# Performance work log

Hardware: AMD Instinct MI355X
Metric: run time of the kernel (lower is better)

The kernel has to match this reference:

```python
import jax, jax.numpy as jnp
import numpy as np

E, T, IN, OUT = 8, 16384, 1024, 1024  # n_groups, total_tokens, in_features, out_features


def setup_inputs() -> dict:
    key = jax.random.key(0)
    kx, kw, ks = jax.random.split(key, 3)
    x = jax.random.normal(kx, (T, IN), dtype=jnp.float32)
    # kaiming_uniform-ish scale for weight [E, OUT, IN]
    weight = jax.random.normal(kw, (E, OUT, IN), dtype=jnp.float32) * (1.0 / np.sqrt(IN))
    # ragged segment lengths that sum exactly to T (random cut points)
    cuts = jnp.sort(jax.random.randint(ks, (E - 1,), 0, T + 1)).astype(jnp.int32)
    seg_lens = jnp.diff(
        jnp.concatenate([jnp.zeros((1,), jnp.int32), cuts, jnp.full((1,), T, jnp.int32)])
    )
    return {"x": x, "weight": weight, "seg_lens": seg_lens}


def reference(x, weight, seg_lens):
    # Grouped GEMM: row t of x is multiplied by weight[g(t)].T where g(t) is the
    # segment (expert) that token t falls into per seg_lens. trans_b=True.
    n_groups = weight.shape[0]
    bounds = jnp.cumsum(seg_lens)                                  # [E]
    seg_id = jnp.searchsorted(bounds, jnp.arange(x.shape[0]), side="right")  # [T]
    y = jnp.zeros((x.shape[0], weight.shape[1]), dtype=x.dtype)
    for e in range(n_groups):  # small fixed loop over groups
        y = y + jnp.where((seg_id == e)[:, None], x @ weight[e].T, 0)
    return y
```

## Files before the change

### kernel.cpp

```cpp
#include <hip/hip_runtime.h>

#define T_TOK  16384
#define IN_F   1024
#define OUT_F  1024
#define NE     8
#define BM     128
#define BN     128
#define BK     32
#define NTHREADS 256
#define ROW_TILE_SLOTS 136

typedef __bf16 bf16;
typedef bf16  bf16x4 __attribute__((ext_vector_type(4)));
typedef bf16  bf16x8 __attribute__((ext_vector_type(8)));
typedef float f32x4  __attribute__((ext_vector_type(4)));

#define NX_ELEM ((size_t)T_TOK * IN_F)
#define NW_ELEM ((size_t)NE * OUT_F * IN_F)
#define WS_NEED ((NX_ELEM + NW_ELEM) * sizeof(bf16))

__global__ __launch_bounds__(NTHREADS)
void cvt_to_bf16(const float* __restrict__ x, const float* __restrict__ w,
                 bf16* __restrict__ xb, bf16* __restrict__ wb)
{
    const size_t NX8 = NX_ELEM / 8;
    const size_t NW8 = NW_ELEM / 8;
    size_t stride = (size_t)gridDim.x * blockDim.x;
    for (size_t i = (size_t)blockIdx.x * blockDim.x + threadIdx.x;
         i < NX8 + NW8; i += stride) {
        const float* src;
        bf16* dst;
        if (i < NX8) { src = x + i * 8;          dst = xb + i * 8; }
        else         { src = w + (i - NX8) * 8;  dst = wb + (i - NX8) * 8; }
        f32x4 v0 = *(const f32x4*)(src);
        f32x4 v1 = *(const f32x4*)(src + 4);
        bf16x8 h;
        #pragma unroll
        for (int j = 0; j < 4; ++j) { h[j] = (bf16)v0[j]; h[4 + j] = (bf16)v1[j]; }
        *(bf16x8*)dst = h;
    }
}

__global__ __launch_bounds__(NTHREADS)
void grouped_gemm_bf16(const bf16* __restrict__ x,
                       const bf16* __restrict__ wgt,
                       const int*  __restrict__ seg_lens,
                       float* __restrict__ out)
{
    __shared__ __align__(16) bf16 As[BM * BK];
    __shared__ __align__(16) bf16 Bs[BN * BK];

    const int m    = blockIdx.y;
    const int col0 = blockIdx.x * BN;

    int e_sel = -1, row0 = 0, rows = 0;
    {
        int start = 0, acct = 0;
        #pragma unroll
        for (int e = 0; e < NE; ++e) {
            int len = seg_lens[e];
            int nt  = (len + BM - 1) >> 7;
            if (e_sel < 0 && m >= acct && m < acct + nt) {
                e_sel = e;
                row0  = start + (m - acct) * BM;
                int rem = start + len - row0;
                rows = rem < BM ? rem : BM;
            }
            acct  += nt;
            start += len;
        }
    }
    if (e_sel < 0) return;

    const int tid  = threadIdx.x;
    const int lane = tid & 63;
    const int wave = tid >> 6;
    const int wm   = (wave >> 1) * 64;
    const int wn   = (wave & 1) * 64;
    const int quad = lane >> 4;
    const int l16  = lane & 15;

    const bf16* wbase = wgt + ((size_t)e_sel * OUT_F + (size_t)col0) * IN_F;

    f32x4 acc[4][4] = {};

    for (int k0 = 0; k0 < IN_F; k0 += BK) {
        __syncthreads();

        #pragma unroll
        for (int t = 0; t < 2; ++t) {
            int c  = t * NTHREADS + tid;
            int rg = row0 + (c >> 2);
            if (rg > T_TOK - 1) rg = T_TOK - 1;
            const bf16* gp = x + (size_t)rg * IN_F + k0 + (c & 3) * 8;
            __builtin_amdgcn_global_load_lds(
                (const __attribute__((address_space(1))) void*)gp,
                (__attribute__((address_space(3))) void*)(&As[c * 8]),
                16, 0, 0);
        }
        #pragma unroll
        for (int t = 0; t < 2; ++t) {
            int c = t * NTHREADS + tid;
            const bf16* gp = wbase + (size_t)(c >> 2) * IN_F + k0 + (c & 3) * 8;
            __builtin_amdgcn_global_load_lds(
                (const __attribute__((address_space(1))) void*)gp,
                (__attribute__((address_space(3))) void*)(&Bs[c * 8]),
                16, 0, 0);
        }
        __syncthreads();

        bf16x8 af[4], bfr[4];
        #pragma unroll
        for (int t = 0; t < 4; ++t)
            af[t] = *(const bf16x8*)(&As[(wm + t * 16 + l16) * BK + quad * 8]);
        #pragma unroll
        for (int u = 0; u < 4; ++u)
            bfr[u] = *(const bf16x8*)(&Bs[(wn + u * 16 + l16) * BK + quad * 8]);

        #pragma unroll
        for (int t = 0; t < 4; ++t)
            #pragma unroll
            for (int u = 0; u < 4; ++u)
                acc[t][u] = __builtin_amdgcn_mfma_f32_16x16x32_bf16(
                    af[t], bfr[u], acc[t][u], 0, 0, 0);
    }

    #pragma unroll
    for (int t = 0; t < 4; ++t) {
        #pragma unroll
        for (int r = 0; r < 4; ++r) {
            int row = wm + t * 16 + quad * 4 + r;
            if (row < rows) {
                size_t ob = (size_t)(row0 + row) * OUT_F + col0;
                #pragma unroll
                for (int u = 0; u < 4; ++u)
                    out[ob + wn + u * 16 + l16] = acc[t][u][r];
            }
        }
    }
}

__global__ __launch_bounds__(NTHREADS)
void grouped_gemm_f32io_fused(const float* __restrict__ x,
                              const float* __restrict__ wgt,
                              const int*  __restrict__ seg_lens,
                              float* __restrict__ out)
{
    __shared__ __align__(16) bf16 As[BM * BK];
    __shared__ __align__(16) bf16 Bs[BN * BK];

    const int m    = blockIdx.y;
    const int col0 = blockIdx.x * BN;

    int e_sel = -1, row0 = 0, rows = 0;
    {
        int start = 0, acct = 0;
        #pragma unroll
        for (int e = 0; e < NE; ++e) {
            int len = seg_lens[e];
            int nt  = (len + BM - 1) >> 7;
            if (e_sel < 0 && m >= acct && m < acct + nt) {
                e_sel = e;
                row0  = start + (m - acct) * BM;
                int rem = start + len - row0;
                rows = rem < BM ? rem : BM;
            }
            acct  += nt;
            start += len;
        }
    }
    if (e_sel < 0) return;

    const int tid  = threadIdx.x;
    const int lane = tid & 63;
    const int wave = tid >> 6;
    const int wm   = (wave >> 1) * 64;
    const int wn   = (wave & 1) * 64;
    const int quad = lane >> 4;
    const int l16  = lane & 15;

    const float* wbase = wgt + ((size_t)e_sel * OUT_F + (size_t)col0) * IN_F;

    f32x4 acc[4][4] = {};

    for (int k0 = 0; k0 < IN_F; k0 += BK) {
        f32x4 a_st[4], b_st[4];
        #pragma unroll
        for (int t = 0; t < 4; ++t) {
            int c  = t * NTHREADS + tid;
            int rg = row0 + (c >> 3);
            if (rg > T_TOK - 1) rg = T_TOK - 1;
            a_st[t] = *(const f32x4*)(x + (size_t)rg * IN_F + k0 + (c & 7) * 4);
            b_st[t] = *(const f32x4*)(wbase + (size_t)(c >> 3) * IN_F + k0 + (c & 7) * 4);
        }
        __syncthreads();
        #pragma unroll
        for (int t = 0; t < 4; ++t) {
            int c = t * NTHREADS + tid;
            bf16x4 ha, hb;
            #pragma unroll
            for (int j = 0; j < 4; ++j) { ha[j] = (bf16)a_st[t][j]; hb[j] = (bf16)b_st[t][j]; }
            *(bf16x4*)(&As[(c >> 3) * BK + (c & 7) * 4]) = ha;
            *(bf16x4*)(&Bs[(c >> 3) * BK + (c & 7) * 4]) = hb;
        }
        __syncthreads();

        bf16x8 af[4], bfr[4];
        #pragma unroll
        for (int t = 0; t < 4; ++t)
            af[t] = *(const bf16x8*)(&As[(wm + t * 16 + l16) * BK + quad * 8]);
        #pragma unroll
        for (int u = 0; u < 4; ++u)
            bfr[u] = *(const bf16x8*)(&Bs[(wn + u * 16 + l16) * BK + quad * 8]);

        #pragma unroll
        for (int t = 0; t < 4; ++t)
            #pragma unroll
            for (int u = 0; u < 4; ++u)
                acc[t][u] = __builtin_amdgcn_mfma_f32_16x16x32_bf16(
                    af[t], bfr[u], acc[t][u], 0, 0, 0);
    }

    #pragma unroll
    for (int t = 0; t < 4; ++t) {
        #pragma unroll
        for (int r = 0; r < 4; ++r) {
            int row = wm + t * 16 + quad * 4 + r;
            if (row < rows) {
                size_t ob = (size_t)(row0 + row) * OUT_F + col0;
                #pragma unroll
                for (int u = 0; u < 4; ++u)
                    out[ob + wn + u * 16 + l16] = acc[t][u][r];
            }
        }
    }
}

extern "C" void kernel_launch(void* const* d_in, const int* in_sizes, int n_in,
                              void* d_out, int out_size, void* d_ws, size_t ws_size,
                              hipStream_t stream) {
    const float* x   = (const float*)d_in[0];
    const float* wgt = (const float*)d_in[1];
    const int*   seg = (const int*)d_in[2];
    float* out = (float*)d_out;

    dim3 block(NTHREADS, 1, 1);
    dim3 grid2(OUT_F / BN, ROW_TILE_SLOTS, 1);

    if (ws_size >= WS_NEED) {
        bf16* xb = (bf16*)d_ws;
        bf16* wb = xb + NX_ELEM;
        cvt_to_bf16<<<3072, block, 0, stream>>>(x, wgt, xb, wb);
        grouped_gemm_bf16<<<grid2, block, 0, stream>>>(xb, wb, seg, out);
    } else {
        grouped_gemm_f32io_fused<<<grid2, block, 0, stream>>>(x, wgt, seg, out);
    }
}
```

Baseline: 217.5 us.

## Convert only weights to bf16 and double-buffer GEMM with in-kernel x conversion

The separate x-to-bf16 pre-pass is dropped, so only the weights are converted in a standalone kernel. The GEMM now reads fp32 x directly, converts it in registers and writes it to LDS. Both A and B tiles are double-buffered so the next tile's global loads overlap the current MFMA work, with one barrier per iteration instead of two. This removes a full 64MB read/32MB write pass over x, but x tiles are now reloaded as fp32 by each of the 8 column blocks, and per-thread register pressure rises.

```diff
diff --git a/kernel.cpp b/kernel.cpp
--- a/kernel.cpp
+++ b/kernel.cpp
@@ -7,6 +7,7 @@
 #define BM     128
 #define BN     128
 #define BK     32
+#define NITER  (IN_F / BK)
 #define NTHREADS 256
 #define ROW_TILE_SLOTS 136
 
@@ -15,40 +16,29 @@
 typedef bf16  bf16x8 __attribute__((ext_vector_type(8)));
 typedef float f32x4  __attribute__((ext_vector_type(4)));
 
-#define NX_ELEM ((size_t)T_TOK * IN_F)
 #define NW_ELEM ((size_t)NE * OUT_F * IN_F)
-#define WS_NEED ((NX_ELEM + NW_ELEM) * sizeof(bf16))
+#define WS_NEED (NW_ELEM * sizeof(bf16))
 
 __global__ __launch_bounds__(NTHREADS)
-void cvt_to_bf16(const float* __restrict__ x, const float* __restrict__ w,
-                 bf16* __restrict__ xb, bf16* __restrict__ wb)
+void cvt_w_bf16(const float* __restrict__ w, bf16* __restrict__ wb)
 {
-    const size_t NX8 = NX_ELEM / 8;
-    const size_t NW8 = NW_ELEM / 8;
-    size_t stride = (size_t)gridDim.x * blockDim.x;
-    for (size_t i = (size_t)blockIdx.x * blockDim.x + threadIdx.x;
-         i < NX8 + NW8; i += stride) {
-        const float* src;
-        bf16* dst;
-        if (i < NX8) { src = x + i * 8;          dst = xb + i * 8; }
-        else         { src = w + (i - NX8) * 8;  dst = wb + (i - NX8) * 8; }
-        f32x4 v0 = *(const f32x4*)(src);
-        f32x4 v1 = *(const f32x4*)(src + 4);
-        bf16x8 h;
-        #pragma unroll
-        for (int j = 0; j < 4; ++j) { h[j] = (bf16)v0[j]; h[4 + j] = (bf16)v1[j]; }
-        *(bf16x8*)dst = h;
-    }
+    size_t i = ((size_t)blockIdx.x * NTHREADS + threadIdx.x) * 8;
+    f32x4 v0 = *(const f32x4*)(w + i);
+    f32x4 v1 = *(const f32x4*)(w + i + 4);
+    bf16x8 h;
+    #pragma unroll
+    for (int j = 0; j < 4; ++j) { h[j] = (bf16)v0[j]; h[4 + j] = (bf16)v1[j]; }
+    *(bf16x8*)(wb + i) = h;
 }
 
 __global__ __launch_bounds__(NTHREADS)
-void grouped_gemm_bf16(const bf16* __restrict__ x,
-                       const bf16* __restrict__ wgt,
+void grouped_gemm_pipe(const float* __restrict__ x,
+                       const bf16* __restrict__ wb,
                        const int*  __restrict__ seg_lens,
                        float* __restrict__ out)
 {
-    __shared__ __align__(16) bf16 As[BM * BK];
-    __shared__ __align__(16) bf16 Bs[BN * BK];
+    __shared__ __align__(16) bf16 As[2][BM * BK];
+    __shared__ __align__(16) bf16 Bs[2][BN * BK];
 
     const int m    = blockIdx.y;
     const int col0 = blockIdx.x * BN;
@@ -80,42 +70,67 @@
     const int quad = lane >> 4;
     const int l16  = lane & 15;
 
-    const bf16* wbase = wgt + ((size_t)e_sel * OUT_F + (size_t)col0) * IN_F;
-
-    f32x4 acc[4][4] = {};
-
-    for (int k0 = 0; k0 < IN_F; k0 += BK) {
-        __syncthreads();
-
+    const int rowA = tid >> 1;
+    const int koff = (tid & 1) * 16;
+    int rgA = row0 + rowA;
+    if (rgA > T_TOK - 1) rgA = T_TOK - 1;
+    const float* aptr = x + (size_t)rgA * IN_F + koff;
+    const int aoff = rowA * BK + koff;
+
+    const bf16* wbase = wb + ((size_t)e_sel * OUT_F + col0) * IN_F;
+
+    {
+        f32x4 a0 = *(const f32x4*)(aptr + 0);
+        f32x4 a1 = *(const f32x4*)(aptr + 4);
+        f32x4 a2 = *(const f32x4*)(aptr + 8);
+        f32x4 a3 = *(const f32x4*)(aptr + 12);
         #pragma unroll
         for (int t = 0; t < 2; ++t) {
-            int c  = t * NTHREADS + tid;
-            int rg = row0 + (c >> 2);
-            if (rg > T_TOK - 1) rg = T_TOK - 1;
-            const bf16* gp = x + (size_t)rg * IN_F + k0 + (c & 3) * 8;
+            int c = t * NTHREADS + tid;
+            const bf16* gp = wbase + (size_t)(c >> 2) * IN_F + (c & 3) * 8;
             __builtin_amdgcn_global_load_lds(
                 (const __attribute__((address_space(1))) void*)gp,
-                (__attribute__((address_space(3))) void*)(&As[c * 8]),
+                (__attribute__((address_space(3))) void*)(&Bs[0][c * 8]),
                 16, 0, 0);
         }
+        bf16x8 h0, h1;
+        #pragma unroll
+        for (int j = 0; j < 4; ++j) {
+            h0[j] = (bf16)a0[j]; h0[4 + j] = (bf16)a1[j];
+            h1[j] = (bf16)a2[j]; h1[4 + j] = (bf16)a3[j];
+        }
+        *(bf16x8*)(&As[0][aoff])     = h0;
+        *(bf16x8*)(&As[0][aoff + 8]) = h1;
+    }
+
+    f32x4 acc[4][4] = {};
+
+    for (int i = 0; i < NITER; ++i) {
+        __syncthreads();
+        const int cur = i & 1, nxt = cur ^ 1;
+        const int kn  = ((i + 1) & (NITER - 1)) * BK;
+
+        f32x4 a0 = *(const f32x4*)(aptr + kn);
+        f32x4 a1 = *(const f32x4*)(aptr + kn + 4);
+        f32x4 a2 = *(const f32x4*)(aptr + kn + 8);
+        f32x4 a3 = *(const f32x4*)(aptr + kn + 12);
         #pragma unroll
         for (int t = 0; t < 2; ++t) {
             int c = t * NTHREADS + tid;
-            const bf16* gp = wbase + (size_t)(c >> 2) * IN_F + k0 + (c & 3) * 8;
+            const bf16* gp = wbase + (size_t)(c >> 2) * IN_F + kn + (c & 3) * 8;
             __builtin_amdgcn_global_load_lds(
                 (const __attribute__((address_space(1))) void*)gp,
-                (__attribute__((address_space(3))) void*)(&Bs[c * 8]),
+                (__attribute__((address_space(3))) void*)(&Bs[nxt][c * 8]),
                 16, 0, 0);
         }
-        __syncthreads();
 
         bf16x8 af[4], bfr[4];
         #pragma unroll
         for (int t = 0; t < 4; ++t)
-            af[t] = *(const bf16x8*)(&As[(wm + t * 16 + l16) * BK + quad * 8]);
+            af[t] = *(const bf16x8*)(&As[cur][(wm + t * 16 + l16) * BK + quad * 8]);
         #pragma unroll
         for (int u = 0; u < 4; ++u)
-            bfr[u] = *(const bf16x8*)(&Bs[(wn + u * 16 + l16) * BK + quad * 8]);
+            bfr[u] = *(const bf16x8*)(&Bs[cur][(wn + u * 16 + l16) * BK + quad * 8]);
 
         #pragma unroll
         for (int t = 0; t < 4; ++t)
@@ -123,6 +138,15 @@
             for (int u = 0; u < 4; ++u)
                 acc[t][u] = __builtin_amdgcn_mfma_f32_16x16x32_bf16(
                     af[t], bfr[u], acc[t][u], 0, 0, 0);
+
+        bf16x8 h0, h1;
+        #pragma unroll
+        for (int j = 0; j < 4; ++j) {
+            h0[j] = (bf16)a0[j]; h0[4 + j] = (bf16)a1[j];
+            h1[j] = (bf16)a2[j]; h1[4 + j] = (bf16)a3[j];
+        }
+        *(bf16x8*)(&As[nxt][aoff])     = h0;
+        *(bf16x8*)(&As[nxt][aoff + 8]) = h1;
     }
 
     #pragma unroll
@@ -248,10 +272,9 @@
     dim3 grid2(OUT_F / BN, ROW_TILE_SLOTS, 1);
 
     if (ws_size >= WS_NEED) {
-        bf16* xb = (bf16*)d_ws;
-        bf16* wb = xb + NX_ELEM;
-        cvt_to_bf16<<<3072, block, 0, stream>>>(x, wgt, xb, wb);
-        grouped_gemm_bf16<<<grid2, block, 0, stream>>>(xb, wb, seg, out);
+        bf16* wb = (bf16*)d_ws;
+        cvt_w_bf16<<<(int)(NW_ELEM / 8 / NTHREADS), block, 0, stream>>>(wgt, wb);
+        grouped_gemm_pipe<<<grid2, block, 0, stream>>>(x, wb, seg, out);
     } else {
         grouped_gemm_f32io_fused<<<grid2, block, 0, stream>>>(x, wgt, seg, out);
     }
```

Result: slower. 227.2 us (+4.4%).

## Restructure bf16 grouped GEMM: 64-row tiles, A direct-to-register, double-buffered swizzled B

Applied to the files above, without the earlier changes.

The bf16 GEMM kernel now uses 64-row tiles (more blocks, less padding waste on ragged segments). The A operand is loaded straight from global memory into registers in MFMA fragment layout, and the B operand is double-buffered in LDS with an XOR swizzle. The next K-slice is prefetched while the current one is computed, which leaves one barrier per iteration instead of two. Smaller tiles raise the global traffic per FLOP and halve MFMA work per wave, and the A loads skip LDS reuse, so each wave reads A rows on its own.

```diff
diff --git a/kernel.cpp b/kernel.cpp
--- a/kernel.cpp
+++ b/kernel.cpp
@@ -4,11 +4,12 @@
 #define IN_F   1024
 #define OUT_F  1024
 #define NE     8
-#define BM     128
+#define BM     64
 #define BN     128
 #define BK     32
+#define NITER  (IN_F / BK)
 #define NTHREADS 256
-#define ROW_TILE_SLOTS 136
+#define ROW_TILE_SLOTS (T_TOK / BM + NE)
 
 typedef __bf16 bf16;
 typedef bf16  bf16x4 __attribute__((ext_vector_type(4)));
@@ -42,13 +43,12 @@
 }
 
 __global__ __launch_bounds__(NTHREADS)
-void grouped_gemm_bf16(const bf16* __restrict__ x,
-                       const bf16* __restrict__ wgt,
-                       const int*  __restrict__ seg_lens,
-                       float* __restrict__ out)
+void grouped_gemm_v6(const bf16* __restrict__ xb,
+                     const bf16* __restrict__ wb,
+                     const int*  __restrict__ seg_lens,
+                     float* __restrict__ out)
 {
-    __shared__ __align__(16) bf16 As[BM * BK];
-    __shared__ __align__(16) bf16 Bs[BN * BK];
+    __shared__ __align__(16) bf16 Bs[2][BN * BK];
 
     const int m    = blockIdx.y;
     const int col0 = blockIdx.x * BN;
@@ -59,12 +59,133 @@
         #pragma unroll
         for (int e = 0; e < NE; ++e) {
             int len = seg_lens[e];
-            int nt  = (len + BM - 1) >> 7;
+            int nt  = (len + BM - 1) >> 6;
             if (e_sel < 0 && m >= acct && m < acct + nt) {
                 e_sel = e;
                 row0  = start + (m - acct) * BM;
                 int rem = start + len - row0;
                 rows = rem < BM ? rem : BM;
+            }
+            acct  += nt;
+            start += len;
+        }
+    }
+    if (e_sel < 0) return;
+
+    const int tid  = threadIdx.x;
+    const int lane = tid & 63;
+    const int wave = tid >> 6;
+    const int wm   = (wave >> 1) * 32;
+    const int wn   = (wave & 1) * 64;
+    const int quad = lane >> 4;
+    const int l16  = lane & 15;
+
+    const bf16* agp[2];
+    #pragma unroll
+    for (int t = 0; t < 2; ++t) {
+        int rg = row0 + wm + t * 16 + l16;
+        if (rg > T_TOK - 1) rg = T_TOK - 1;
+        agp[t] = xb + (size_t)rg * IN_F + quad * 8;
+    }
+
+    const bf16* bgp[2];
+    int ldsoff[2];
+    #pragma unroll
+    for (int t = 0; t < 2; ++t) {
+        int c    = t * NTHREADS + tid;
+        int rowB = c >> 2;
+        int q    = (c & 3) ^ ((rowB >> 1) & 3);
+        bgp[t]    = wb + ((size_t)e_sel * OUT_F + col0 + rowB) * IN_F + q * 8;
+        ldsoff[t] = c * 8;
+    }
+
+    int boff[4];
+    #pragma unroll
+    for (int u = 0; u < 4; ++u) {
+        int row = wn + u * 16 + l16;
+        boff[u] = row * BK + ((quad ^ ((row >> 1) & 3)) * 8);
+    }
+
+    bf16x8 apf[2];
+    apf[0] = *(const bf16x8*)(agp[0]);
+    apf[1] = *(const bf16x8*)(agp[1]);
+    #pragma unroll
+    for (int t = 0; t < 2; ++t)
+        __builtin_amdgcn_global_load_lds(
+            (const __attribute__((address_space(1))) void*)bgp[t],
+            (__attribute__((address_space(3))) void*)(&Bs[0][ldsoff[t]]),
+            16, 0, 0);
+
+    f32x4 acc[2][4] = {};
+
+    for (int i = 0; i < NITER; ++i) {
+        __syncthreads();
+        const int cur = i & 1, nxt = cur ^ 1;
+        const int kn  = ((i + 1) & (NITER - 1)) * BK;
+
+        bf16x8 a0 = apf[0], a1 = apf[1];
+
+        apf[0] = *(const bf16x8*)(agp[0] + kn);
+        apf[1] = *(const bf16x8*)(agp[1] + kn);
+        #pragma unroll
+        for (int t = 0; t < 2; ++t)
+            __builtin_amdgcn_global_load_lds(
+                (const __attribute__((address_space(1))) void*)(bgp[t] + kn),
+                (__attribute__((address_space(3))) void*)(&Bs[nxt][ldsoff[t]]),
+                16, 0, 0);
+
+        bf16x8 bfr[4];
+        #pragma unroll
+        for (int u = 0; u < 4; ++u)
+            bfr[u] = *(const bf16x8*)(&Bs[cur][boff[u]]);
+
+        #pragma unroll
+        for (int u = 0; u < 4; ++u) {
+            acc[0][u] = __builtin_amdgcn_mfma_f32_16x16x32_bf16(a0, bfr[u], acc[0][u], 0, 0, 0);
+            acc[1][u] = __builtin_amdgcn_mfma_f32_16x16x32_bf16(a1, bfr[u], acc[1][u], 0, 0, 0);
+        }
+    }
+
+    #pragma unroll
+    for (int t = 0; t < 2; ++t) {
+        #pragma unroll
+        for (int r = 0; r < 4; ++r) {
+            int row = wm + t * 16 + quad * 4 + r;
+            if (row < rows) {
+                size_t ob = (size_t)(row0 + row) * OUT_F + col0;
+                #pragma unroll
+                for (int u = 0; u < 4; ++u)
+                    out[ob + wn + u * 16 + l16] = acc[t][u][r];
+            }
+        }
+    }
+}
+
+#define FBM 128
+__global__ __launch_bounds__(NTHREADS)
+void grouped_gemm_f32io_fused(const float* __restrict__ x,
+                              const float* __restrict__ wgt,
+                              const int*  __restrict__ seg_lens,
+                              float* __restrict__ out)
+{
+    __shared__ __align__(16) bf16 As[FBM * BK];
+    __shared__ __align__(16) bf16 Bsf[BN * BK];
+
+    const int m    = blockIdx.y;
+    const int col0 = blockIdx.x * BN;
+
+    int e_sel = -1, row0 = 0, rows = 0;
+    {
+        int start = 0, acct = 0;
+        #pragma unroll
+        for (int e = 0; e < NE; ++e) {
+            int len = seg_lens[e];
+            int nt  = (len + FBM - 1) >> 7;
+            if (e_sel < 0 && m >= acct && m < acct + nt) {
+                e_sel = e;
+                row0  = start + (m - acct) * FBM;
+                int rem = start + len - row0;
+                rows = rem < FBM ? rem : FBM;
             }
             acct  += nt;
             start += len;
@@ -80,32 +201,29 @@
     const int quad = lane >> 4;
     const int l16  = lane & 15;
 
-    const bf16* wbase = wgt + ((size_t)e_sel * OUT_F + (size_t)col0) * IN_F;
+    const float* wbase = wgt + ((size_t)e_sel * OUT_F + (size_t)col0) * IN_F;
 
     f32x4 acc[4][4] = {};
 
     for (int k0 = 0; k0 < IN_F; k0 += BK) {
+        f32x4 a_st[4], b_st[4];
+        #pragma unroll
+        for (int t = 0; t < 4; ++t) {
+            int c  = t * NTHREADS + tid;
+            int rg = row0 + (c >> 3);
+            if (rg > T_TOK - 1) rg = T_TOK - 1;
+            a_st[t] = *(const f32x4*)(x + (size_t)rg * IN_F + k0 + (c & 7) * 4);
+            b_st[t] = *(const f32x4*)(wbase + (size_t)(c >> 3) * IN_F + k0 + (c & 7) * 4);
+        }
         __syncthreads();
-
-        #pragma unroll
-        for (int t = 0; t < 2; ++t) {
-            int c  = t * NTHREADS + tid;
-            int rg = row0 + (c >> 2);
-            if (rg > T_TOK - 1) rg = T_TOK - 1;
-            const bf16* gp = x + (size_t)rg * IN_F + k0 + (c & 3) * 8;
-            __builtin_amdgcn_global_load_lds(
-                (const __attribute__((address_space(1))) void*)gp,
-                (__attribute__((address_space(3))) void*)(&As[c * 8]),
-                16, 0, 0);
-        }
-        #pragma unroll
-        for (int t = 0; t < 2; ++t) {
+        #pragma unroll
+        for (int t = 0; t < 4; ++t) {
             int c = t * NTHREADS + tid;
-            const bf16* gp = wbase + (size_t)(c >> 2) * IN_F + k0 + (c & 3) * 8;
-            __builtin_amdgcn_global_load_lds(
-                (const __attribute__((address_space(1))) void*)gp,
-                (__attribute__((address_space(3))) void*)(&Bs[c * 8]),
-                16, 0, 0);
+            bf16x4 ha, hb;
+            #pragma unroll
+            for (int j = 0; j < 4; ++j) { ha[j] = (bf16)a_st[t][j]; hb[j] = (bf16)b_st[t][j]; }
+            *(bf16x4*)(&As[(c >> 3) * BK + (c & 7) * 4]) = ha;
+            *(bf16x4*)(&Bsf[(c >> 3) * BK + (c & 7) * 4]) = hb;
         }
         __syncthreads();
 
@@ -115,7 +233,7 @@
             af[t] = *(const bf16x8*)(&As[(wm + t * 16 + l16) * BK + quad * 8]);
         #pragma unroll
         for (int u = 0; u < 4; ++u)
-            bfr[u] = *(const bf16x8*)(&Bs[(wn + u * 16 + l16) * BK + quad * 8]);
+            bfr[u] = *(const bf16x8*)(&Bsf[(wn + u * 16 + l16) * BK + quad * 8]);
 
         #pragma unroll
         for (int t = 0; t < 4; ++t)
@@ -140,102 +258,6 @@
     }
 }
 
-__global__ __launch_bounds__(NTHREADS)
-void grouped_gemm_f32io_fused(const float* __restrict__ x,
-                              const float* __restrict__ wgt,
-                              const int*  __restrict__ seg_lens,
-                              float* __restrict__ out)
-{
-    __shared__ __align__(16) bf16 As[BM * BK];
-    __shared__ __align__(16) bf16 Bs[BN * BK];
-
-    const int m    = blockIdx.y;
-    const int col0 = blockIdx.x * BN;
-
-    int e_sel = -1, row0 = 0, rows = 0;
-    {
-        int start = 0, acct = 0;
-        #pragma unroll
-        for (int e = 0; e < NE; ++e) {
-            int len = seg_lens[e];
-            int nt  = (len + BM - 1) >> 7;
-            if (e_sel < 0 && m >= acct && m < acct + nt) {
-                e_sel = e;
-                row0  = start + (m - acct) * BM;
-                int rem = start + len - row0;
-                rows = rem < BM ? rem : BM;
-            }
-            acct  += nt;
-            start += len;
-        }
-    }
-    if (e_sel < 0) return;
-
-    const int tid  = threadIdx.x;
-    const int lane = tid & 63;
-    const int wave = tid >> 6;
-    const int wm   = (wave >> 1) * 64;
-    const int wn   = (wave & 1) * 64;
-    const int quad = lane >> 4;
-    const int l16  = lane & 15;
-
-    const float* wbase = wgt + ((size_t)e_sel * OUT_F + (size_t)col0) * IN_F;
-
-    f32x4 acc[4][4] = {};
-
-    for (int k0 = 0; k0 < IN_F; k0 += BK) {
-        f32x4 a_st[4], b_st[4];
-        #pragma unroll
-        for (int t = 0; t < 4; ++t) {
-            int c  = t * NTHREADS + tid;
-            int rg = row0 + (c >> 3);
-            if (rg > T_TOK - 1) rg = T_TOK - 1;
-            a_st[t] = *(const f32x4*)(x + (size_t)rg * IN_F + k0 + (c & 7) * 4);
-            b_st[t] = *(const f32x4*)(wbase + (size_t)(c >> 3) * IN_F + k0 + (c & 7) * 4);
-        }
-        __syncthreads();
-        #pragma unroll
-        for (int t = 0; t < 4; ++t) {
-            int c = t * NTHREADS + tid;
-            bf16x4 ha, hb;
-            #pragma unroll
-            for (int j = 0; j < 4; ++j) { ha[j] = (bf16)a_st[t][j]; hb[j] = (bf16)b_st[t][j]; }
-            *(bf16x4*)(&As[(c >> 3) * BK + (c & 7) * 4]) = ha;
-            *(bf16x4*)(&Bs[(c >> 3) * BK + (c & 7) * 4]) = hb;
-        }
-        __syncthreads();
-
-        bf16x8 af[4], bfr[4];
-        #pragma unroll
-        for (int t = 0; t < 4; ++t)
-            af[t] = *(const bf16x8*)(&As[(wm + t * 16 + l16) * BK + quad * 8]);
-        #pragma unroll
-        for (int u = 0; u < 4; ++u)
-            bfr[u] = *(const bf16x8*)(&Bs[(wn + u * 16 + l16) * BK + quad * 8]);
-
-        #pragma unroll
-        for (int t = 0; t < 4; ++t)
-            #pragma unroll
-            for (int u = 0; u < 4; ++u)
-                acc[t][u] = __builtin_amdgcn_mfma_f32_16x16x32_bf16(
-                    af[t], bfr[u], acc[t][u], 0, 0, 0);
-    }
-
-    #pragma unroll
-    for (int t = 0; t < 4; ++t) {
-        #pragma unroll
-        for (int r = 0; r < 4; ++r) {
-            int row = wm + t * 16 + quad * 4 + r;
-            if (row < rows) {
-                size_t ob = (size_t)(row0 + row) * OUT_F + col0;
-                #pragma unroll
-                for (int u = 0; u < 4; ++u)
-                    out[ob + wn + u * 16 + l16] = acc[t][u][r];
-            }
-        }
-    }
-}
-
 extern "C" void kernel_launch(void* const* d_in, const int* in_sizes, int n_in,
                               void* d_out, int out_size, void* d_ws, size_t ws_size,
                               hipStream_t stream) {
@@ -245,14 +267,15 @@
     float* out = (float*)d_out;
 
     dim3 block(NTHREADS, 1, 1);
-    dim3 grid2(OUT_F / BN, ROW_TILE_SLOTS, 1);
 
     if (ws_size >= WS_NEED) {
         bf16* xb = (bf16*)d_ws;
         bf16* wb = xb + NX_ELEM;
         cvt_to_bf16<<<3072, block, 0, stream>>>(x, wgt, xb, wb);
-        grouped_gemm_bf16<<<grid2, block, 0, stream>>>(xb, wb, seg, out);
+        dim3 grid2(OUT_F / BN, ROW_TILE_SLOTS, 1);
+        grouped_gemm_v6<<<grid2, block, 0, stream>>>(xb, wb, seg, out);
     } else {
-        grouped_gemm_f32io_fused<<<grid2, block, 0, stream>>>(x, wgt, seg, out);
-    }
-}
+        dim3 gridf(OUT_F / BN, T_TOK / FBM + NE, 1);
+        grouped_gemm_f32io_fused<<<gridf, block, 0, stream>>>(x, wgt, seg, out);
+    }
+}
```

Measured after the change: 235.2 us. 8.2% more time.
